# Kernel tuning notes

Hardware: AMD Instinct MI355X
Metric: run time of the kernel (lower is better)

The kernel has to match this reference:

```python
import jax, jax.numpy as jnp
import numpy as np

N = 50000
E = 800000
NFEAT = 128
NHID = 128
NCLASS = 8
BN_EPS = 1e-5
NORM_EPS = 1e-12


def _xavier(key, out_f, in_f):
    lim = float(np.sqrt(6.0 / (in_f + out_f)))
    return jax.random.uniform(key, (out_f, in_f), jnp.float32, -lim, lim)


def setup_inputs() -> dict:
    key = jax.random.key(0)
    ks = jax.random.split(key, 10)
    x = jax.random.normal(ks[0], (N, NFEAT), jnp.float32)
    edge_index = jax.random.randint(ks[1], (2, E), 0, N, jnp.int64)
    return {
        "x": x,
        "edge_index": edge_index,
        # conv1: lin_l (neighbor branch, has bias), lin_r (root branch, no bias)
        "W1l": _xavier(ks[2], NHID, NFEAT),
        "b1l": jnp.zeros((NHID,), jnp.float32),
        "W1r": _xavier(ks[3], NHID, NFEAT),
        # BatchNorm1d(nhid)
        "bn_gamma": jnp.ones((NHID,), jnp.float32),
        "bn_beta": jnp.zeros((NHID,), jnp.float32),
        # conv2
        "W2l": _xavier(ks[4], NHID, NHID),
        "b2l": jnp.zeros((NHID,), jnp.float32),
        "W2r": _xavier(ks[5], NHID, NHID),
        # fc
        "Wfc": _xavier(ks[6], NCLASS, NHID),
        "bfc": jnp.zeros((NCLASS,), jnp.float32),
    }


def _sage_conv(x, src, dst, inv_deg, Wl, bl, Wr):
    # gather neighbor features along edges, scatter-mean into destination nodes
    msg = x[src]                                            # [E, F]
    agg = jax.ops.segment_sum(msg, dst, num_segments=N)      # [N, F]
    agg = agg * inv_deg[:, None]                             # mean aggregation
    out = agg @ Wl.T + bl + x @ Wr.T                         # lin_l(agg) + lin_r(x)
    # L2 normalize per node (normalize=True)
    norm = jnp.sqrt(jnp.sum(out * out, axis=-1, keepdims=True))
    return out / jnp.maximum(norm, NORM_EPS)


def reference(x, edge_index, W1l, b1l, W1r, bn_gamma, bn_beta, W2l, b2l, W2r, Wfc, bfc):
    src, dst = edge_index[0], edge_index[1]
    deg = jax.ops.segment_sum(jnp.ones((E,), x.dtype), dst, num_segments=N)
    inv_deg = jnp.where(deg > 0, 1.0 / jnp.maximum(deg, 1.0), 0.0)

    h = _sage_conv(x, src, dst, inv_deg, W1l, b1l, W1r)

    # transition: ReLU -> BatchNorm1d (batch stats, biased var) -> Dropout (identity, eval)
    h = jax.nn.relu(h)
    mu = jnp.mean(h, axis=0)
    var = jnp.mean((h - mu) ** 2, axis=0)
    h = (h - mu) * jax.lax.rsqrt(var + BN_EPS) * bn_gamma + bn_beta

    h = _sage_conv(h, src, dst, inv_deg, W2l, b2l, W2r)
    return h @ Wfc.T + bfc
```

## Files before the change

### kernel.cpp

```cpp
#include <hip/hip_runtime.h>
#include <hip/hip_bf16.h>

#define NF 128
#define CAP 64

typedef float f4 __attribute__((ext_vector_type(4)));
typedef short s16x8 __attribute__((ext_vector_type(8)));
typedef unsigned short u16x8 __attribute__((ext_vector_type(8)));

static __device__ __forceinline__ unsigned short f2b(float f) {
    union { float f; unsigned u; } c; c.f = f;
    unsigned r = c.u + 0x7fffu + ((c.u >> 16) & 1u);
    return (unsigned short)(r >> 16);
}
static __device__ __forceinline__ float blo(unsigned v) { return __uint_as_float(v << 16); }
static __device__ __forceinline__ float bhi(unsigned v) { return __uint_as_float(v & 0xffff0000u); }

__global__ __launch_bounds__(256) void k_prep(int* __restrict__ zp, int nwords, int ZB,
                                              int SB,
                                              unsigned* __restrict__ csr32, int csrWords,
                                              const float* __restrict__ x,
                                              unsigned* __restrict__ out32, int N,
                                              const float* __restrict__ w0,
                                              const float* __restrict__ w1,
                                              const float* __restrict__ w2,
                                              unsigned short* __restrict__ wt) {
    int b = blockIdx.x;
    int S = N + 1;
    int CV2 = (S * 64 + 255) / 256;
    if (b < ZB) {
        int i = b * 256 + threadIdx.x;
        if (i < nwords) zp[i] = 0;
    } else if (b < ZB + SB) {
        int i = (b - ZB) * 256 + threadIdx.x;
        unsigned sv = ((unsigned)N << 16) | (unsigned)N;
        if (i < csrWords) csr32[i] = sv;
    } else if (b < ZB + SB + CV2) {
        int i = (b - ZB - SB) * 256 + threadIdx.x;
        if (i >= S * 64) return;
        int n = i >> 6, l = i & 63;
        int s = l >> 4, li = l & 15;
        unsigned pv = 0;
        if (n < N) {
            float2 v = *(const float2*)(x + (size_t)n * NF + l * 2);
            pv = (unsigned)f2b(v.x) | ((unsigned)f2b(v.y) << 16);
        }
        out32[(size_t)s * S * 16 + (size_t)n * 16 + li] = pv;
    } else {
        int t = (b - ZB - SB - CV2) * 256 + threadIdx.x;
        if (t >= 6144) return;
        int mat = t >> 11, rem = t & 2047;
        int col = rem >> 4, ks = (rem >> 2) & 3, qq = rem & 3;
        const float* W = (mat == 0) ? w0 : (mat == 1) ? w1 : w2;
        int layer = (mat == 2) ? 1 : 0, half = (mat == 1) ? 1 : 0;
        const float* src = W + col * NF + ks * 32 + qq * 8;
        u16x8 d;
#pragma unroll
        for (int j = 0; j < 8; ++j) d[j] = f2b(src[j]);
        *(u16x8*)(wt + layer * 65536 + (half * 4 + ks) * 4096 + (col >> 4) * 512 +
                  (qq * 16 + (col & 15)) * 8) = d;
    }
}

__global__ __launch_bounds__(256) void k_fill(const int* __restrict__ ei, int E,
                                              int* __restrict__ cnt,
                                              unsigned short* __restrict__ csr,
                                              int nper) {
    int b = blockIdx.x;
    int i = (b >> 3) * 256 + threadIdx.x;
    if (i >= E) return;
    int d = ei[E + i];
    int lo = (b & 7) * nper;
    if (d >= lo && d < lo + nper) {
        int p = atomicAdd(&cnt[d], 1);
        csr[(size_t)d * CAP + p] = (unsigned short)ei[i];
    }
}

__global__ __launch_bounds__(256) void k_prep_w2(const float* __restrict__ bnSum,
                                                 const float* __restrict__ bnSq,
                                                 const float* __restrict__ gamma,
                                                 const float* __restrict__ beta,
                                                 const float* __restrict__ w2r,
                                                 const float* __restrict__ b2l,
                                                 unsigned short* __restrict__ wtL2,
                                                 float* __restrict__ bias2,
                                                 float* __restrict__ sbn,
                                                 float* __restrict__ bbn, float n) {
    __shared__ float sl[128], bl[128];
    int tid = threadIdx.x;
    if (tid < 128) {
        float su = 0.f, sq = 0.f;
#pragma unroll
        for (int s = 0; s < 8; ++s) { su += bnSum[s * 128 + tid]; sq += bnSq[s * 128 + tid]; }
        float mu = su / n;
        float var = fmaxf(sq / n - mu * mu, 0.f);
        float s = gamma[tid] / sqrtf(var + 1e-5f);
        sl[tid] = s;
        bl[tid] = beta[tid] - mu * s;
    }
    __syncthreads();
    if (blockIdx.x < 8) {
        int t = blockIdx.x * 256 + tid;
        int col = t >> 4, ks = (t >> 2) & 3, qq = t & 3;
        int k0 = ks * 32 + qq * 8;
        u16x8 d;
#pragma unroll
        for (int j = 0; j < 8; ++j) d[j] = f2b(w2r[col * NF + k0 + j] * sl[k0 + j]);
        *(u16x8*)(wtL2 + (4 + ks) * 4096 + (col >> 4) * 512 +
                  (qq * 16 + (col & 15)) * 8) = d;
    } else {
        if (tid < NF) {
            float s = b2l[tid];
            for (int k = 0; k < NF; ++k) s += w2r[tid * NF + k] * bl[k];
            bias2[tid] = s;
            sbn[tid] = sl[tid];
            bbn[tid] = bl[tid];
        }
    }
}

template <bool TR>
__global__ __launch_bounds__(256) void k_agg(const uint4* __restrict__ T4all,
                                             const unsigned short* __restrict__ csr,
                                             const int* __restrict__ deg,
                                             const float* __restrict__ sbn,
                                             const float* __restrict__ bbn,
                                             uint4* __restrict__ outT4, int N) {
    int b = blockIdx.x;
    int S = N + 1;
    int s = (b & 7) >> 1;
    int chunk = (b >> 3) * 2 + (b & 1);
    int tid = threadIdx.x;
    int wid = tid >> 6, lane = tid & 63, g = lane >> 4, li = lane & 15;
    int node = chunk * 16 + wid * 4 + g;
    if (node >= N) return;
    int cnt = deg[node];
    int cntR = (cnt + 15) & ~15;
    int nb = li >> 2, fq = li & 3;
    const uint4* T4 = T4all + (size_t)s * S * 4;
    const unsigned short* cp = csr + (size_t)node * CAP;
    float a0 = 0, a1 = 0, a2 = 0, a3 = 0, a4 = 0, a5 = 0, a6 = 0, a7 = 0;
    for (int j = 0; j < cntR; j += 16) {
        int sA = cp[j + nb], sB = cp[j + 4 + nb], sC = cp[j + 8 + nb], sD = cp[j + 12 + nb];
        uint4 vA = T4[(size_t)sA * 4 + fq];
        uint4 vB = T4[(size_t)sB * 4 + fq];
        uint4 vC = T4[(size_t)sC * 4 + fq];
        uint4 vD = T4[(size_t)sD * 4 + fq];
        a0 += (blo(vA.x) + blo(vB.x)) + (blo(vC.x) + blo(vD.x));
        a1 += (bhi(vA.x) + bhi(vB.x)) + (bhi(vC.x) + bhi(vD.x));
        a2 += (blo(vA.y) + blo(vB.y)) + (blo(vC.y) + blo(vD.y));
        a3 += (bhi(vA.y) + bhi(vB.y)) + (bhi(vC.y) + bhi(vD.y));
        a4 += (blo(vA.z) + blo(vB.z)) + (blo(vC.z) + blo(vD.z));
        a5 += (bhi(vA.z) + bhi(vB.z)) + (bhi(vC.z) + bhi(vD.z));
        a6 += (blo(vA.w) + blo(vB.w)) + (blo(vC.w) + blo(vD.w));
        a7 += (bhi(vA.w) + bhi(vB.w)) + (bhi(vC.w) + bhi(vD.w));
    }
    a0 += __shfl_xor(a0, 4); a1 += __shfl_xor(a1, 4);
    a2 += __shfl_xor(a2, 4); a3 += __shfl_xor(a3, 4);
    a4 += __shfl_xor(a4, 4); a5 += __shfl_xor(a5, 4);
    a6 += __shfl_xor(a6, 4); a7 += __shfl_xor(a7, 4);
    a0 += __shfl_xor(a0, 8); a1 += __shfl_xor(a1, 8);
    a2 += __shfl_xor(a2, 8); a3 += __shfl_xor(a3, 8);
    a4 += __shfl_xor(a4, 8); a5 += __shfl_xor(a5, 8);
    a6 += __shfl_xor(a6, 8); a7 += __shfl_xor(a7, 8);
    if (li < 4) {
        float id = (cnt > 0) ? 1.0f / (float)cnt : 0.f;
        float r[8] = {a0 * id, a1 * id, a2 * id, a3 * id,
                      a4 * id, a5 * id, a6 * id, a7 * id};
        if (TR) {
            if (cnt > 0) {
                const float2* sc2 = (const float2*)(sbn + s * 32 + fq * 8);
                const float2* bc2 = (const float2*)(bbn + s * 32 + fq * 8);
#pragma unroll
                for (int i = 0; i < 4; ++i) {
                    float2 sc = sc2[i], bc = bc2[i];
                    r[2 * i]     = r[2 * i]     * sc.x + bc.x;
                    r[2 * i + 1] = r[2 * i + 1] * sc.y + bc.y;
                }
            }
        }
        uint4 p;
        p.x = (unsigned)f2b(r[0]) | ((unsigned)f2b(r[1]) << 16);
        p.y = (unsigned)f2b(r[2]) | ((unsigned)f2b(r[3]) << 16);
        p.z = (unsigned)f2b(r[4]) | ((unsigned)f2b(r[5]) << 16);
        p.w = (unsigned)f2b(r[6]) | ((unsigned)f2b(r[7]) << 16);
        outT4[((size_t)s * S + node) * 4 + fq] = p;
    }
}

template <int MODE>
__global__ __launch_bounds__(256, 4) void k_lin(
    const unsigned short* __restrict__ aggB,
    const unsigned short* __restrict__ src2,
    const unsigned short* __restrict__ wt,
    const float* __restrict__ bias,
    const float* __restrict__ wfc, const float* __restrict__ bfc,
    unsigned short* __restrict__ outb,
    float* __restrict__ outf,
    float* __restrict__ bnSum, float* __restrict__ bnSq, int N) {
    __shared__ __align__(16) unsigned short wlds[16384];
    __shared__ float sbuf[1024];

    int tid = threadIdx.x;
    int S = N + 1;
    int lane = tid & 63;
    int q = lane >> 4, m = lane & 15;
    int wv = tid >> 6;
    int row_base = blockIdx.x * 64 + wv * 16;

    int r = row_base + m; if (r >= N) r = N - 1;
    size_t rr = (size_t)r * 32 + q * 8;
    s16x8 afr[8];
#pragma unroll
    for (int ks = 0; ks < 4; ++ks)
        afr[ks] = *(const s16x8*)(aggB + (size_t)ks * S * 32 + rr);
#pragma unroll
    for (int ks = 0; ks < 4; ++ks)
        afr[4 + ks] = *(const s16x8*)(src2 + (size_t)ks * S * 32 + rr);

    if constexpr (MODE == 1) {
        if (tid < 256) sbuf[tid] = 0.f;
    } else {
        *(f4*)&sbuf[tid * 4] = ((const f4*)wfc)[tid];
    }

    f4 acc[8];
#pragma unroll
    for (int c = 0; c < 8; ++c) acc[c] = (f4){0.f, 0.f, 0.f, 0.f};

    const unsigned short* wb = wlds + lane * 8;
#pragma unroll
    for (int h = 0; h < 2; ++h) {
        const f4* wsrc4 = (const f4*)(wt + h * 16384);
        f4* wd4 = (f4*)wlds;
#pragma unroll
        for (int it = 0; it < 8; ++it) wd4[tid + it * 256] = wsrc4[tid + it * 256];
        __syncthreads();
#pragma unroll
        for (int ks = 0; ks < 4; ++ks) {
#pragma unroll
            for (int c = 0; c < 8; ++c) {
                s16x8 bfr = *(const s16x8*)(wb + ks * 4096 + c * 512);
                acc[c] = __builtin_amdgcn_mfma_f32_16x16x32_bf16(afr[h * 4 + ks], bfr,
                                                                 acc[c], 0, 0, 0);
            }
        }
        __syncthreads();
    }

#pragma unroll
    for (int c = 0; c < 8; ++c) {
        float b = bias[c * 16 + m];
#pragma unroll
        for (int i = 0; i < 4; ++i) acc[c][i] += b;
    }
    float ss[4];
#pragma unroll
    for (int i = 0; i < 4; ++i) {
        float s = 0.f;
#pragma unroll
        for (int c = 0; c < 8; ++c) s += acc[c][i] * acc[c][i];
        s += __shfl_xor(s, 1); s += __shfl_xor(s, 2);
        s += __shfl_xor(s, 4); s += __shfl_xor(s, 8);
        ss[i] = 1.0f / fmaxf(sqrtf(s), 1e-12f);
    }
#pragma unroll
    for (int c = 0; c < 8; ++c)
#pragma unroll
        for (int i = 0; i < 4; ++i) acc[c][i] *= ss[i];

    if constexpr (MODE == 1) {
#pragma unroll
        for (int c = 0; c < 8; ++c)
#pragma unroll
            for (int i = 0; i < 4; ++i) acc[c][i] = fmaxf(acc[c][i], 0.f);
#pragma unroll
        for (int i = 0; i < 4; ++i) {
            int row = row_base + q * 4 + i;
            if (row <= N) {
#pragma unroll
                for (int c = 0; c < 8; ++c)
                    outb[(size_t)(c >> 1) * S * 32 + (size_t)row * 32 + (c & 1) * 16 + m] =
                        (row < N) ? f2b(acc[c][i]) : (unsigned short)0;
            }
        }
        float su[8], sq[8];
#pragma unroll
        for (int c = 0; c < 8; ++c) { su[c] = 0.f; sq[c] = 0.f; }
#pragma unroll
        for (int i = 0; i < 4; ++i) {
            bool vi = (row_base + q * 4 + i) < N;
#pragma unroll
            for (int c = 0; c < 8; ++c) {
                float u = vi ? acc[c][i] : 0.f;
                su[c] += u; sq[c] += u * u;
            }
        }
#pragma unroll
        for (int c = 0; c < 8; ++c) {
            su[c] += __shfl_xor(su[c], 16); su[c] += __shfl_xor(su[c], 32);
            sq[c] += __shfl_xor(sq[c], 16); sq[c] += __shfl_xor(sq[c], 32);
        }
        if (lane < 16) {
#pragma unroll
            for (int c = 0; c < 8; ++c) {
                atomicAdd(&sbuf[c * 16 + m], su[c]);
                atomicAdd(&sbuf[128 + c * 16 + m], sq[c]);
            }
        }
        __syncthreads();
        int shard = (blockIdx.x & 7) * 128;
        if (tid < 128)      atomicAdd(&bnSum[shard + tid], sbuf[tid]);
        else if (tid < 256) atomicAdd(&bnSq[shard + tid - 128], sbuf[tid]);
    } else {
        float o[8][4];
#pragma unroll
        for (int cls = 0; cls < 8; ++cls)
#pragma unroll
            for (int i = 0; i < 4; ++i) o[cls][i] = 0.f;
#pragma unroll
        for (int cls = 0; cls < 8; ++cls) {
#pragma unroll
            for (int c = 0; c < 8; ++c) {
                float wv2 = sbuf[cls * NF + c * 16 + m];
#pragma unroll
                for (int i = 0; i < 4; ++i) o[cls][i] += acc[c][i] * wv2;
            }
#pragma unroll
            for (int i = 0; i < 4; ++i) {
                float tt = o[cls][i];
                tt += __shfl_xor(tt, 1); tt += __shfl_xor(tt, 2);
                tt += __shfl_xor(tt, 4); tt += __shfl_xor(tt, 8);
                o[cls][i] = tt;
            }
        }
        float sel[4] = {0.f, 0.f, 0.f, 0.f};
#pragma unroll
        for (int cls = 0; cls < 8; ++cls) {
            bool p = (m == cls);
#pragma unroll
            for (int i = 0; i < 4; ++i) sel[i] = p ? o[cls][i] : sel[i];
        }
        if (m < 8) {
            float bb = bfc[m];
#pragma unroll
            for (int i = 0; i < 4; ++i) {
                int row = row_base + q * 4 + i;
                if (row < N) outf[(size_t)row * 8 + m] = sel[i] + bb;
            }
        }
    }
}

extern "C" void kernel_launch(void* const* d_in, const int* in_sizes, int n_in,
                              void* d_out, int out_size, void* d_ws, size_t ws_size,
                              hipStream_t stream) {
    const float* x   = (const float*)d_in[0];
    const int*   ei  = (const int*)d_in[1];
    const float* W1l = (const float*)d_in[2];
    const float* b1l = (const float*)d_in[3];
    const float* W1r = (const float*)d_in[4];
    const float* gam = (const float*)d_in[5];
    const float* bet = (const float*)d_in[6];
    const float* W2l = (const float*)d_in[7];
    const float* b2l = (const float*)d_in[8];
    const float* W2r = (const float*)d_in[9];
    const float* Wfc = (const float*)d_in[10];
    const float* bfc = (const float*)d_in[11];
    int N = in_sizes[0] / NF;
    int E = in_sizes[1] / 2;
    int S = N + 1;

    char* w = (char*)d_ws;
    size_t o = 0;
#define ALO(nbytes) (o = (o + 255) & ~(size_t)255, o += (nbytes), (w + o - (nbytes)))
    int* cnt    = (int*)ALO((size_t)N * 4);
    float* bnSum = (float*)ALO(4096);
    float* bnSq  = (float*)ALO(4096);
    size_t zwords = o / 4;
    unsigned short* csr = (unsigned short*)ALO((size_t)N * CAP * 2);
    unsigned short* wt  = (unsigned short*)ALO((size_t)2 * 65536 * 2);
    float* sbn   = (float*)ALO(512);
    float* bbn   = (float*)ALO(512);
    float* bias2 = (float*)ALO(512);
    unsigned short* xb   = (unsigned short*)ALO((size_t)S * NF * 2);
    unsigned short* aggB = (unsigned short*)ALO((size_t)S * NF * 2);
    unsigned short* h1b  = (unsigned short*)ALO((size_t)S * NF * 2);
#undef ALO
    (void)ws_size; (void)n_in; (void)out_size;

    int EB8 = ((E + 255) / 256) * 8;
    int nper = (N + 7) / 8;
    int aggBlocks = ((N + 31) / 32) * 8;
    int LB = (N + 63) / 64;
    int CV2 = (S * 64 + 255) / 256;
    int ZB = (int)((zwords + 255) / 256);
    int csrWords = N * CAP / 2;
    int SB = (csrWords + 255) / 256;

    k_prep<<<ZB + SB + CV2 + 24, 256, 0, stream>>>((int*)d_ws, (int)zwords, ZB, SB,
                                                   (unsigned*)csr, csrWords,
                                                   x, (unsigned*)xb, N, W1l, W1r, W2l, wt);
    k_fill<<<EB8, 256, 0, stream>>>(ei, E, cnt, csr, nper);

    k_agg<false><<<aggBlocks, 256, 0, stream>>>((const uint4*)xb, csr, cnt,
                                                nullptr, nullptr, (uint4*)aggB, N);
    k_lin<1><<<LB, 256, 0, stream>>>(aggB, xb, wt, b1l, nullptr, nullptr,
                                     h1b, nullptr, bnSum, bnSq, N);
    k_prep_w2<<<9, 256, 0, stream>>>(bnSum, bnSq, gam, bet, W2r, b2l,
                                     wt + 65536, bias2, sbn, bbn, (float)N);
    k_agg<true><<<aggBlocks, 256, 0, stream>>>((const uint4*)h1b, csr, cnt,
                                               sbn, bbn, (uint4*)aggB, N);
    k_lin<2><<<LB, 256, 0, stream>>>(aggB, h1b, wt + 65536, bias2, Wfc, bfc,
                                     nullptr, (float*)d_out, nullptr, nullptr, N);
}
```

Measured before the change: 150.9 us.

## Fold BatchNorm into layer-2 linear kernel and drop separate weight-prep launch

Removes the k_prep_w2 kernel, which folded the BatchNorm scale into W2r and computed a fused bias. Instead, the raw W2r is converted to bf16 in k_prep, and each k_lin<2> block recomputes the BN statistics and applies the affine transform to its A-fragments in registers before the MFMA loop. Aggregated rows are gated by degree so that empty neighborhoods stay zero. This saves one kernel launch and simplifies k_agg. The cost is a per-block BN reduction, an extra __syncthreads, and a second bf16 rounding on the normalized activations.

```diff
diff --git a/kernel.cpp b/kernel.cpp
--- a/kernel.cpp
+++ b/kernel.cpp
@@ -15,6 +15,9 @@
 }
 static __device__ __forceinline__ float blo(unsigned v) { return __uint_as_float(v << 16); }
 static __device__ __forceinline__ float bhi(unsigned v) { return __uint_as_float(v & 0xffff0000u); }
+static __device__ __forceinline__ float b2f(unsigned short v) {
+    return __uint_as_float((unsigned)v << 16);
+}
 
 __global__ __launch_bounds__(256) void k_prep(int* __restrict__ zp, int nwords, int ZB,
                                               int SB,
@@ -24,6 +27,7 @@
                                               const float* __restrict__ w0,
                                               const float* __restrict__ w1,
                                               const float* __restrict__ w2,
+                                              const float* __restrict__ w3,
                                               unsigned short* __restrict__ wt) {
     int b = blockIdx.x;
     int S = N + 1;
@@ -48,11 +52,11 @@
         out32[(size_t)s * S * 16 + (size_t)n * 16 + li] = pv;
     } else {
         int t = (b - ZB - SB - CV2) * 256 + threadIdx.x;
-        if (t >= 6144) return;
+        if (t >= 8192) return;
         int mat = t >> 11, rem = t & 2047;
         int col = rem >> 4, ks = (rem >> 2) & 3, qq = rem & 3;
-        const float* W = (mat == 0) ? w0 : (mat == 1) ? w1 : w2;
-        int layer = (mat == 2) ? 1 : 0, half = (mat == 1) ? 1 : 0;
+        const float* W = (mat == 0) ? w0 : (mat == 1) ? w1 : (mat == 2) ? w2 : w3;
+        int layer = mat >> 1, half = mat & 1;
         const float* src = W + col * NF + ks * 32 + qq * 8;
         u16x8 d;
 #pragma unroll
@@ -77,55 +81,9 @@
     }
 }
 
-__global__ __launch_bounds__(256) void k_prep_w2(const float* __restrict__ bnSum,
-                                                 const float* __restrict__ bnSq,
-                                                 const float* __restrict__ gamma,
-                                                 const float* __restrict__ beta,
-                                                 const float* __restrict__ w2r,
-                                                 const float* __restrict__ b2l,
-                                                 unsigned short* __restrict__ wtL2,
-                                                 float* __restrict__ bias2,
-                                                 float* __restrict__ sbn,
-                                                 float* __restrict__ bbn, float n) {
-    __shared__ float sl[128], bl[128];
-    int tid = threadIdx.x;
-    if (tid < 128) {
-        float su = 0.f, sq = 0.f;
-#pragma unroll
-        for (int s = 0; s < 8; ++s) { su += bnSum[s * 128 + tid]; sq += bnSq[s * 128 + tid]; }
-        float mu = su / n;
-        float var = fmaxf(sq / n - mu * mu, 0.f);
-        float s = gamma[tid] / sqrtf(var + 1e-5f);
-        sl[tid] = s;
-        bl[tid] = beta[tid] - mu * s;
-    }
-    __syncthreads();
-    if (blockIdx.x < 8) {
-        int t = blockIdx.x * 256 + tid;
-        int col = t >> 4, ks = (t >> 2) & 3, qq = t & 3;
-        int k0 = ks * 32 + qq * 8;
-        u16x8 d;
-#pragma unroll
-        for (int j = 0; j < 8; ++j) d[j] = f2b(w2r[col * NF + k0 + j] * sl[k0 + j]);
-        *(u16x8*)(wtL2 + (4 + ks) * 4096 + (col >> 4) * 512 +
-                  (qq * 16 + (col & 15)) * 8) = d;
-    } else {
-        if (tid < NF) {
-            float s = b2l[tid];
-            for (int k = 0; k < NF; ++k) s += w2r[tid * NF + k] * bl[k];
-            bias2[tid] = s;
-            sbn[tid] = sl[tid];
-            bbn[tid] = bl[tid];
-        }
-    }
-}
-
-template <bool TR>
 __global__ __launch_bounds__(256) void k_agg(const uint4* __restrict__ T4all,
                                              const unsigned short* __restrict__ csr,
                                              const int* __restrict__ deg,
-                                             const float* __restrict__ sbn,
-                                             const float* __restrict__ bbn,
                                              uint4* __restrict__ outT4, int N) {
     int b = blockIdx.x;
     int S = N + 1;
@@ -166,25 +124,11 @@
     a6 += __shfl_xor(a6, 8); a7 += __shfl_xor(a7, 8);
     if (li < 4) {
         float id = (cnt > 0) ? 1.0f / (float)cnt : 0.f;
-        float r[8] = {a0 * id, a1 * id, a2 * id, a3 * id,
-                      a4 * id, a5 * id, a6 * id, a7 * id};
-        if (TR) {
-            if (cnt > 0) {
-                const float2* sc2 = (const float2*)(sbn + s * 32 + fq * 8);
-                const float2* bc2 = (const float2*)(bbn + s * 32 + fq * 8);
-#pragma unroll
-                for (int i = 0; i < 4; ++i) {
-                    float2 sc = sc2[i], bc = bc2[i];
-                    r[2 * i]     = r[2 * i]     * sc.x + bc.x;
-                    r[2 * i + 1] = r[2 * i + 1] * sc.y + bc.y;
-                }
-            }
-        }
         uint4 p;
-        p.x = (unsigned)f2b(r[0]) | ((unsigned)f2b(r[1]) << 16);
-        p.y = (unsigned)f2b(r[2]) | ((unsigned)f2b(r[3]) << 16);
-        p.z = (unsigned)f2b(r[4]) | ((unsigned)f2b(r[5]) << 16);
-        p.w = (unsigned)f2b(r[6]) | ((unsigned)f2b(r[7]) << 16);
+        p.x = (unsigned)f2b(a0 * id) | ((unsigned)f2b(a1 * id) << 16);
+        p.y = (unsigned)f2b(a2 * id) | ((unsigned)f2b(a3 * id) << 16);
+        p.z = (unsigned)f2b(a4 * id) | ((unsigned)f2b(a5 * id) << 16);
+        p.w = (unsigned)f2b(a6 * id) | ((unsigned)f2b(a7 * id) << 16);
         outT4[((size_t)s * S + node) * 4 + fq] = p;
     }
 }
@@ -198,9 +142,13 @@
     const float* __restrict__ wfc, const float* __restrict__ bfc,
     unsigned short* __restrict__ outb,
     float* __restrict__ outf,
-    float* __restrict__ bnSum, float* __restrict__ bnSq, int N) {
+    float* __restrict__ bnSum, float* __restrict__ bnSq,
+    const float* __restrict__ gam, const float* __restrict__ bet,
+    const int* __restrict__ degArr,
+    int N) {
     __shared__ __align__(16) unsigned short wlds[16384];
     __shared__ float sbuf[1024];
+    __shared__ float snb[256];
 
     int tid = threadIdx.x;
     int S = N + 1;
@@ -223,6 +171,39 @@
         if (tid < 256) sbuf[tid] = 0.f;
     } else {
         *(f4*)&sbuf[tid * 4] = ((const f4*)wfc)[tid];
+        if (tid < 128) {
+            float su = 0.f, sq = 0.f;
+#pragma unroll
+            for (int s2 = 0; s2 < 8; ++s2) {
+                su += bnSum[s2 * 128 + tid];
+                sq += bnSq[s2 * 128 + tid];
+            }
+            float n = (float)N;
+            float mu = su / n;
+            float var = fmaxf(sq / n - mu * mu, 0.f);
+            float sc = gam[tid] / sqrtf(var + 1e-5f);
+            snb[tid] = sc;
+            snb[128 + tid] = bet[tid] - mu * sc;
+        }
+    }
+
+    if constexpr (MODE == 2) {
+        __syncthreads();
+        bool gate = degArr[r] > 0;
+#pragma unroll
+        for (int ks = 0; ks < 4; ++ks) {
+#pragma unroll
+            for (int j = 0; j < 8; ++j) {
+                int k = ks * 32 + q * 8 + j;
+                float s = snb[k], b = snb[128 + k];
+                float va = b2f((unsigned short)afr[ks][j]);
+                va = gate ? (va * s + b) : 0.f;
+                afr[ks][j] = (short)f2b(va);
+                float vb = b2f((unsigned short)afr[4 + ks][j]);
+                vb = vb * s + b;
+                afr[4 + ks][j] = (short)f2b(vb);
+            }
+        }
     }
 
     f4 acc[8];
@@ -381,9 +362,6 @@
     size_t zwords = o / 4;
     unsigned short* csr = (unsigned short*)ALO((size_t)N * CAP * 2);
     unsigned short* wt  = (unsigned short*)ALO((size_t)2 * 65536 * 2);
-    float* sbn   = (float*)ALO(512);
-    float* bbn   = (float*)ALO(512);
-    float* bias2 = (float*)ALO(512);
     unsigned short* xb   = (unsigned short*)ALO((size_t)S * NF * 2);
     unsigned short* aggB = (unsigned short*)ALO((size_t)S * NF * 2);
     unsigned short* h1b  = (unsigned short*)ALO((size_t)S * NF * 2);
@@ -399,19 +377,18 @@
     int csrWords = N * CAP / 2;
     int SB = (csrWords + 255) / 256;
 
-    k_prep<<<ZB + SB + CV2 + 24, 256, 0, stream>>>((int*)d_ws, (int)zwords, ZB, SB,
+    k_prep<<<ZB + SB + CV2 + 32, 256, 0, stream>>>((int*)d_ws, (int)zwords, ZB, SB,
                                                    (unsigned*)csr, csrWords,
-                                                   x, (unsigned*)xb, N, W1l, W1r, W2l, wt);
+                                                   x, (unsigned*)xb, N,
+                                                   W1l, W1r, W2l, W2r, wt);
     k_fill<<<EB8, 256, 0, stream>>>(ei, E, cnt, csr, nper);
 
-    k_agg<false><<<aggBlocks, 256, 0, stream>>>((const uint4*)xb, csr, cnt,
-                                                nullptr, nullptr, (uint4*)aggB, N);
+    k_agg<<<aggBlocks, 256, 0, stream>>>((const uint4*)xb, csr, cnt, (uint4*)aggB, N);
     k_lin<1><<<LB, 256, 0, stream>>>(aggB, xb, wt, b1l, nullptr, nullptr,
-                                     h1b, nullptr, bnSum, bnSq, N);
-    k_prep_w2<<<9, 256, 0, stream>>>(bnSum, bnSq, gam, bet, W2r, b2l,
-                                     wt + 65536, bias2, sbn, bbn, (float)N);
-    k_agg<true><<<aggBlocks, 256, 0, stream>>>((const uint4*)h1b, csr, cnt,
-                                               sbn, bbn, (uint4*)aggB, N);
-    k_lin<2><<<LB, 256, 0, stream>>>(aggB, h1b, wt + 65536, bias2, Wfc, bfc,
-                                     nullptr, (float*)d_out, nullptr, nullptr, N);
-}
+                                     h1b, nullptr, bnSum, bnSq,
+                                     nullptr, nullptr, nullptr, N);
+    k_agg<<<aggBlocks, 256, 0, stream>>>((const uint4*)h1b, csr, cnt, (uint4*)aggB, N);
+    k_lin<2><<<LB, 256, 0, stream>>>(aggB, h1b, wt + 65536, b2l, Wfc, bfc,
+                                     nullptr, (float*)d_out, bnSum, bnSq,
+                                     gam, bet, cnt, N);
+}
```

Measured after the change: 148.7 us. Within noise of the previous version (-1.5%).
